# Kernel optimization log

Measured on AMD Instinct MI355X. Metric: run time of the kernel, lower is better.

## Reference

```python
import jax, jax.numpy as jnp
import numpy as np

EPS = 1e-6
NUM_HEADS = 16

def rmsnorm(x, w):
    # x: [..., d], w: [d]
    norm = jax.lax.rsqrt(jnp.mean(x * x, axis=-1, keepdims=True) + EPS)
    return w * (x * norm)

def setup_inputs() -> dict:
    key = jax.random.key(0)
    ks = jax.random.split(key, 6)
    B, N, C = 2, 2048, 1024
    H = NUM_HEADS
    hd = C // H
    x = jax.random.normal(ks[0], (B, N, C), dtype=jnp.float32)
    scale = 1.0 / np.sqrt(C)
    qkv_w = jax.random.normal(ks[1], (C, 3 * C), dtype=jnp.float32) * scale
    qkv_b = jnp.zeros((3 * C,), dtype=jnp.float32)
    q_norm_w = jnp.ones((hd,), dtype=jnp.float32)
    k_norm_w = jnp.ones((hd,), dtype=jnp.float32)
    proj_w = jax.random.normal(ks[2], (C, C), dtype=jnp.float32) * scale
    proj_b = jnp.zeros((C,), dtype=jnp.float32)
    return {"x": x, "qkv_w": qkv_w, "qkv_b": qkv_b,
            "q_norm_w": q_norm_w, "k_norm_w": k_norm_w,
            "proj_w": proj_w, "proj_b": proj_b}

def reference(x, qkv_w, qkv_b, q_norm_w, k_norm_w, proj_w, proj_b):
    B, N, C = x.shape
    H = NUM_HEADS
    hd = C // H
    qkv = x @ qkv_w + qkv_b                       # [B,N,3C]
    qkv = qkv.reshape(B, N, 3, H, hd)
    q, k, v = qkv[:, :, 0], qkv[:, :, 1], qkv[:, :, 2]  # [B,N,H,hd]
    q = jnp.transpose(q, (0, 2, 1, 3))            # [B,H,N,hd]
    k = jnp.transpose(k, (0, 2, 1, 3))
    v = jnp.transpose(v, (0, 2, 1, 3))
    q = rmsnorm(q, q_norm_w)
    k = rmsnorm(k, k_norm_w)
    scores = jnp.einsum('bhqd,bhkd->bhqk', q, k) / jnp.sqrt(jnp.float32(hd))
    attn = jax.nn.softmax(scores, axis=-1)
    out = jnp.einsum('bhqk,bhkd->bhqd', attn, v)  # [B,H,N,hd]
    out = jnp.transpose(out, (0, 2, 1, 3)).reshape(B, N, C)
    return out @ proj_w + proj_b
```

## Files before the change

kernel.cpp:

```cpp
#include <hip/hip_runtime.h>

typedef unsigned short u16;
typedef unsigned int u32;
typedef __bf16 bf16x8 __attribute__((ext_vector_type(8)));
typedef float f32x4 __attribute__((ext_vector_type(4)));
typedef unsigned short u16x8 __attribute__((ext_vector_type(8)));
typedef unsigned short u16x4 __attribute__((ext_vector_type(4)));
typedef float f4 __attribute__((ext_vector_type(4)));

__device__ __forceinline__ float bf2f(u16 u) {
    union { unsigned int i; float f; } c; c.i = ((unsigned int)u) << 16; return c.f;
}
__device__ __forceinline__ u16 f2bf(float f) {
    union { float f; unsigned int i; } c; c.f = f;
    unsigned int r = c.i + 0x7FFFu + ((c.i >> 16) & 1u);
    return (u16)(r >> 16);
}
__device__ __forceinline__ u16 f2bf_rtz(float f) {
    union { float f; unsigned int i; } c; c.f = f;
    return (u16)(c.i >> 16);
}
__device__ __forceinline__ float fast_exp2(float x) {
#if __has_builtin(__builtin_amdgcn_exp2f)
    return __builtin_amdgcn_exp2f(x);
#else
    return exp2f(x);
#endif
}
__device__ __forceinline__ void async16(const void* g, void* l) {
    __builtin_amdgcn_global_load_lds(
        (const __attribute__((address_space(1))) u32*)g,
        (__attribute__((address_space(3))) u32*)l, 16, 0, 0);
}

__global__ __launch_bounds__(256) void cast_bf16(
    const float* __restrict__ X, u16* __restrict__ H)
{
    const size_t i = ((size_t)blockIdx.x * 256 + threadIdx.x) * 8;
    u16x8 h;
    #pragma unroll
    for (int e = 0; e < 8; ++e) h[e] = f2bf(X[i + e]);
    *(u16x8*)&H[i] = h;
}

__global__ __launch_bounds__(256) void transpose_cast(
    const float* __restrict__ W, u16* __restrict__ Th, int K, int N)
{
    __shared__ float tile[32][33];
    const int bk = blockIdx.y * 32, bn = blockIdx.x * 32;
    const int tx = threadIdx.x & 31, ty = threadIdx.x >> 5;
    #pragma unroll
    for (int r = ty; r < 32; r += 8)
        tile[r][tx] = W[(size_t)(bk + r) * N + bn + tx];
    __syncthreads();
    #pragma unroll
    for (int r = ty; r < 32; r += 8)
        Th[(size_t)(bn + r) * K + bk + tx] = f2bf(tile[tx][r]);
}

__global__ __launch_bounds__(256) void gemm_qkv(
    const u16* __restrict__ AH, const u16* __restrict__ BH,
    const float* __restrict__ bias,
    u16* __restrict__ Qb, u16* __restrict__ Kb, u16* __restrict__ Vt,
    const float* __restrict__ qw, const float* __restrict__ kw)
{
    const int M = 4096, N = 3072, K = 1024; (void)M; (void)N;
    __shared__ __align__(16) u16 AhT[128 * 32];
    __shared__ __align__(16) u16 BhT[128 * 32];
    const int t = threadIdx.x;
    const int bm = blockIdx.y * 128, bn = blockIdx.x * 128;
    const int wave = t >> 6, lane = t & 63;
    const int wm = (wave >> 1) * 64, wn = (wave & 1) * 64;
    const int l15 = lane & 15, quad = lane >> 4;
    const int srow = lane >> 2, scol = (lane & 3) * 8;

    f32x4 acc[4][4];
    const f32x4 zero = {0.0f, 0.0f, 0.0f, 0.0f};
    #pragma unroll
    for (int i = 0; i < 4; ++i)
        #pragma unroll
        for (int j = 0; j < 4; ++j) acc[i][j] = zero;

    for (int k0 = 0; k0 < K; k0 += 32) {
        #pragma unroll
        for (int rr = 0; rr < 2; ++rr) {
            const int r0 = (rr * 4 + wave) * 16;
            const size_t ga = (size_t)(bm + r0 + srow) * K + k0 + scol;
            const size_t gb = (size_t)(bn + r0 + srow) * K + k0 + scol;
            async16(&AH[ga], &AhT[r0 * 32]);
            async16(&BH[gb], &BhT[r0 * 32]);
        }
        __syncthreads();
        bf16x8 ah[4], bh[4];
        #pragma unroll
        for (int i = 0; i < 4; ++i)
            ah[i] = *(const bf16x8*)&AhT[(wm + i * 16 + l15) * 32 + quad * 8];
        #pragma unroll
        for (int j = 0; j < 4; ++j)
            bh[j] = *(const bf16x8*)&BhT[(wn + j * 16 + l15) * 32 + quad * 8];
        #pragma unroll
        for (int i = 0; i < 4; ++i)
            #pragma unroll
            for (int j = 0; j < 4; ++j)
                acc[i][j] = __builtin_amdgcn_mfma_f32_16x16x32_bf16(
                    ah[i], bh[j], acc[i][j], 0, 0, 0);
        __syncthreads();
    }

    const int gc0 = bn + wn;
    const int sec = gc0 >> 10;
    const int h = (gc0 & 1023) >> 6;
    const int b = bm >> 11;
    const int bhd = b * 16 + h;
    float bv[4], wj[4];
    #pragma unroll
    for (int j = 0; j < 4; ++j) {
        const int d = j * 16 + l15;
        bv[j] = bias[gc0 + d];
        wj[j] = (sec == 2) ? 0.0f : (sec ? kw[d] : qw[d] * 0.18033688011f);
    }
    if (sec < 2) {
        u16* dst = sec ? Kb : Qb;
        #pragma unroll
        for (int i = 0; i < 4; ++i) {
            float val[4][4];
            float ss[4] = {0.0f, 0.0f, 0.0f, 0.0f};
            #pragma unroll
            for (int j = 0; j < 4; ++j)
                #pragma unroll
                for (int r = 0; r < 4; ++r) {
                    val[j][r] = acc[i][j][r] + bv[j];
                    ss[r] += val[j][r] * val[j][r];
                }
            #pragma unroll
            for (int r = 0; r < 4; ++r) {
                #pragma unroll
                for (int m = 1; m < 16; m <<= 1)
                    ss[r] += __shfl_xor(ss[r], m, 64);
                const float nrm = rsqrtf(ss[r] * 0.015625f + 1e-6f);
                const int n = (bm + wm + i * 16 + quad * 4 + r) & 2047;
                const size_t rowb = ((size_t)bhd * 2048 + n) * 64;
                #pragma unroll
                for (int j = 0; j < 4; ++j)
                    dst[rowb + j * 16 + l15] = f2bf(val[j][r] * nrm * wj[j]);
            }
        }
    } else {
        #pragma unroll
        for (int i = 0; i < 4; ++i) {
            const int n0 = (bm + wm + i * 16 + quad * 4) & 2047;
            #pragma unroll
            for (int j = 0; j < 4; ++j) {
                const int d = j * 16 + l15;
                u16x4 pk;
                #pragma unroll
                for (int r = 0; r < 4; ++r)
                    pk[r] = f2bf(acc[i][j][r] + bv[j]);
                *(u16x4*)&Vt[((size_t)bhd * 64 + d) * 2048 + n0] = pk;
            }
        }
    }
}

__global__ __launch_bounds__(256) void gemm_proj(
    const u16* __restrict__ AH, const u16* __restrict__ BH,
    const float* __restrict__ bias, float* __restrict__ C)
{
    const int N = 1024, K = 1024;
    __shared__ __align__(16) u16 AhT[64 * 32];
    __shared__ __align__(16) u16 BhT[128 * 32];
    const int t = threadIdx.x;
    const int bm = blockIdx.y * 64, bn = blockIdx.x * 128;
    const int wave = t >> 6, lane = t & 63;
    const int l15 = lane & 15, quad = lane >> 4;
    const int srow = lane >> 2, scol = (lane & 3) * 8;

    f32x4 acc[4][2];
    const f32x4 zero = {0.0f, 0.0f, 0.0f, 0.0f};
    #pragma unroll
    for (int i = 0; i < 4; ++i)
        #pragma unroll
        for (int j = 0; j < 2; ++j) acc[i][j] = zero;

    for (int k0 = 0; k0 < K; k0 += 32) {
        {
            const int r0 = wave * 16;
            async16(&AH[(size_t)(bm + r0 + srow) * K + k0 + scol],
                    &AhT[r0 * 32]);
        }
        #pragma unroll
        for (int cc = 0; cc < 2; ++cc) {
            const int r0 = (wave * 2 + cc) * 16;
            async16(&BH[(size_t)(bn + r0 + srow) * K + k0 + scol],
                    &BhT[r0 * 32]);
        }
        __syncthreads();
        bf16x8 ah[4], bh[2];
        #pragma unroll
        for (int i = 0; i < 4; ++i)
            ah[i] = *(const bf16x8*)&AhT[(i * 16 + l15) * 32 + quad * 8];
        #pragma unroll
        for (int j = 0; j < 2; ++j)
            bh[j] = *(const bf16x8*)
                &BhT[(wave * 32 + j * 16 + l15) * 32 + quad * 8];
        #pragma unroll
        for (int i = 0; i < 4; ++i)
            #pragma unroll
            for (int j = 0; j < 2; ++j)
                acc[i][j] = __builtin_amdgcn_mfma_f32_16x16x32_bf16(
                    ah[i], bh[j], acc[i][j], 0, 0, 0);
        __syncthreads();
    }

    #pragma unroll
    for (int j = 0; j < 2; ++j) {
        const int col = bn + wave * 32 + j * 16 + l15;
        const float bv = bias[col];
        #pragma unroll
        for (int i = 0; i < 4; ++i) {
            const int row = bm + i * 16 + quad * 4;
            #pragma unroll
            for (int r = 0; r < 4; ++r)
                C[(size_t)(row + r) * N + col] = acc[i][j][r] + bv;
        }
    }
}

__global__ __launch_bounds__(256) void flash_attn_mfma(
    const u16* __restrict__ Qb, const u16* __restrict__ Kb,
    const u16* __restrict__ Vt, float* __restrict__ Opart,
    float* __restrict__ Lpart)
{
    __shared__ __align__(16) u16 Qlds[128 * 64];
    __shared__ __align__(16) u16 Klds[64 * 64];
    __shared__ __align__(16) u16 Vlds[64 * 64];
    __shared__ u16 Plds[128][72];

    const int t = threadIdx.x;
    const int qt = blockIdx.x;
    const int bh = blockIdx.y;
    const int z = blockIdx.z;
    const int n0 = qt * 128;
    const size_t qbase = ((size_t)bh * 2048 + n0) * 64;
    const size_t kbase = (size_t)bh * 2048 * 64;
    const size_t vbase = (size_t)bh * 64 * 2048;
    const int wave = t >> 6, lane = t & 63;
    const int l15 = lane & 15, quad = lane >> 4;
    const int srow8 = lane >> 3;
    const int sgrp = lane & 7;

    #pragma unroll
    for (int c = 0; c < 4; ++c) {
        const int r0 = wave * 32 + c * 8;
        const int row = r0 + srow8;
        const int gg = sgrp ^ (row & 7);
        async16(&Qb[qbase + (size_t)row * 64 + gg * 8], &Qlds[r0 * 64]);
    }
    __syncthreads();

    int kofs[4][2];
    #pragma unroll
    for (int nt = 0; nt < 4; ++nt) {
        const int row = nt * 16 + l15;
        kofs[nt][0] = row * 64 + ((quad ^ (row & 7)) * 8);
        kofs[nt][1] = row * 64 + (((quad + 4) ^ (row & 7)) * 8);
    }
    bf16x8 qf[2][2];
    #pragma unroll
    for (int qs = 0; qs < 2; ++qs) {
        const int row = wave * 32 + qs * 16 + l15;
        qf[qs][0] = *(const bf16x8*)&Qlds[row * 64 + ((quad ^ (row & 7)) * 8)];
        qf[qs][1] = *(const bf16x8*)&Qlds[row * 64 + (((quad + 4) ^ (row & 7)) * 8)];
    }

    f32x4 o[2][4];
    const f32x4 zero = {0.0f, 0.0f, 0.0f, 0.0f};
    #pragma unroll
    for (int qs = 0; qs < 2; ++qs)
        #pragma unroll
        for (int dt = 0; dt < 4; ++dt) o[qs][dt] = zero;
    float lsum[2][4] = {};

    for (int kt = 0; kt < 16; ++kt) {
        const int ktG = z * 16 + kt;
        __syncthreads();
        #pragma unroll
        for (int cc = 0; cc < 2; ++cc) {
            const int r0 = (wave + cc * 4) * 8;
            const int row = r0 + srow8;
            const int gg = sgrp ^ (row & 7);
            async16(&Kb[kbase + (size_t)(ktG * 64 + row) * 64 + gg * 8],
                    &Klds[r0 * 64]);
            async16(&Vt[vbase + (size_t)row * 2048 + ktG * 64 + gg * 8],
                    &Vlds[r0 * 64]);
        }
        __syncthreads();

        f32x4 s[2][4];
        #pragma unroll
        for (int nt = 0; nt < 4; ++nt) {
            bf16x8 kf0 = *(const bf16x8*)&Klds[kofs[nt][0]];
            bf16x8 kf1 = *(const bf16x8*)&Klds[kofs[nt][1]];
            #pragma unroll
            for (int qs = 0; qs < 2; ++qs) {
                s[qs][nt] = zero;
                s[qs][nt] = __builtin_amdgcn_mfma_f32_16x16x32_bf16(
                    qf[qs][0], kf0, s[qs][nt], 0, 0, 0);
                s[qs][nt] = __builtin_amdgcn_mfma_f32_16x16x32_bf16(
                    qf[qs][1], kf1, s[qs][nt], 0, 0, 0);
            }
        }

        #pragma unroll
        for (int qs = 0; qs < 2; ++qs) {
            const int prow = wave * 32 + qs * 16 + quad * 4;
            #pragma unroll
            for (int nt = 0; nt < 4; ++nt)
                #pragma unroll
                for (int r = 0; r < 4; ++r) {
                    const float p = fast_exp2(s[qs][nt][r]);
                    lsum[qs][r] += p;
                    Plds[prow + r][nt * 16 + l15] = f2bf_rtz(p);
                }
        }

        bf16x8 pf[2][2];
        #pragma unroll
        for (int qs = 0; qs < 2; ++qs) {
            const int prow = wave * 32 + qs * 16 + l15;
            pf[qs][0] = *(const bf16x8*)&Plds[prow][quad * 8];
            pf[qs][1] = *(const bf16x8*)&Plds[prow][quad * 8 + 32];
        }

        #pragma unroll
        for (int dt = 0; dt < 4; ++dt) {
            bf16x8 vf0 = *(const bf16x8*)&Vlds[kofs[dt][0]];
            bf16x8 vf1 = *(const bf16x8*)&Vlds[kofs[dt][1]];
            #pragma unroll
            for (int qs = 0; qs < 2; ++qs) {
                o[qs][dt] = __builtin_amdgcn_mfma_f32_16x16x32_bf16(
                    pf[qs][0], vf0, o[qs][dt], 0, 0, 0);
                o[qs][dt] = __builtin_amdgcn_mfma_f32_16x16x32_bf16(
                    pf[qs][1], vf1, o[qs][dt], 0, 0, 0);
            }
        }
    }

    #pragma unroll
    for (int qs = 0; qs < 2; ++qs)
        #pragma unroll
        for (int r = 0; r < 4; ++r) {
            #pragma unroll
            for (int m = 1; m < 16; m <<= 1)
                lsum[qs][r] += __shfl_xor(lsum[qs][r], m, 64);
        }
    const int b = bh >> 4, h = bh & 15;
    const size_t obase =
        ((size_t)z * 4096 + b * 2048 + n0) * 1024 + h * 64;
    const size_t lbase = (size_t)z * 32 * 2048 + (size_t)bh * 2048 + n0;
    #pragma unroll
    for (int qs = 0; qs < 2; ++qs)
        #pragma unroll
        for (int r = 0; r < 4; ++r) {
            const int rofs = wave * 32 + qs * 16 + quad * 4 + r;
            if (l15 == 0) Lpart[lbase + rofs] = lsum[qs][r];
            const size_t rbase = obase + (size_t)rofs * 1024;
            #pragma unroll
            for (int dt = 0; dt < 4; ++dt)
                Opart[rbase + dt * 16 + l15] = o[qs][dt][r];
        }
}

__global__ __launch_bounds__(256) void attn_combine(
    const float* __restrict__ Opart, const float* __restrict__ Lpart,
    u16* __restrict__ Attn)
{
    const int row = blockIdx.x;
    const int t = threadIdx.x;
    const int col = t * 4;
    const int b = row >> 11, n = row & 2047;
    const int h = col >> 6;
    const int bh = b * 16 + h;
    const float l0 = Lpart[(size_t)bh * 2048 + n];
    const float l1 = Lpart[65536 + (size_t)bh * 2048 + n];
    const float inv = 1.0f / (l0 + l1);
    const size_t idx = (size_t)row * 1024 + col;
    f4 o0 = *(const f4*)&Opart[idx];
    f4 o1 = *(const f4*)&Opart[4194304 + idx];
    u16x4 pk;
    #pragma unroll
    for (int e = 0; e < 4; ++e) pk[e] = f2bf((o0[e] + o1[e]) * inv);
    *(u16x4*)&Attn[idx] = pk;
}

extern "C" void kernel_launch(void* const* d_in, const int* in_sizes, int n_in,
                              void* d_out, int out_size, void* d_ws, size_t ws_size,
                              hipStream_t stream)
{
    const float* x      = (const float*)d_in[0];
    const float* qkv_w  = (const float*)d_in[1];
    const float* qkv_b  = (const float*)d_in[2];
    const float* q_nw   = (const float*)d_in[3];
    const float* k_nw   = (const float*)d_in[4];
    const float* proj_w = (const float*)d_in[5];
    const float* proj_b = (const float*)d_in[6];
    float* out = (float*)d_out;

    char* ws = (char*)d_ws;
    u16* AttnB  = (u16*)ws;
    u16* qwT    = (u16*)(ws + 8388608);
    u16* pwT    = (u16*)(ws + 14680064);
    u16* Xb     = (u16*)(ws + 16777216);
    float* Lp   = (float*)(ws + 16777216);
    u16* QbB    = (u16*)(ws + 25165824);
    u16* KbB    = (u16*)(ws + 33554432);
    u16* VtB    = (u16*)(ws + 41943040);
    float* Op   = (float*)(ws + 50331648);
    (void)in_sizes; (void)n_in; (void)out_size;
    if (ws_size < 83886080u) return;

    cast_bf16<<<dim3(2048), 256, 0, stream>>>(x, Xb);
    transpose_cast<<<dim3(3072 / 32, 1024 / 32), 256, 0, stream>>>(
        qkv_w, qwT, 1024, 3072);
    transpose_cast<<<dim3(1024 / 32, 1024 / 32), 256, 0, stream>>>(
        proj_w, pwT, 1024, 1024);
    gemm_qkv<<<dim3(3072 / 128, 4096 / 128), 256, 0, stream>>>(
        Xb, qwT, qkv_b, QbB, KbB, VtB, q_nw, k_nw);
    flash_attn_mfma<<<dim3(16, 32, 2), 256, 0, stream>>>(
        QbB, KbB, VtB, Op, Lp);
    attn_combine<<<dim3(4096), 256, 0, stream>>>(Op, Lp, AttnB);
    gemm_proj<<<dim3(1024 / 128, 4096 / 64), 256, 0, stream>>>(
        AttnB, pwT, proj_b, out);
}
```

Before: 211.8 us.

## Drop split-K attention and fuse softmax normalization into flash kernel epilogue

The flash attention kernel no longer splits the key range across two z-blocks. Each block now walks all 32 key tiles and normalizes its output in the epilogue using row sums gathered through shared memory, then writes bf16 directly. This removes the fp32 partial-output writes, the Lpart buffer and the separate combine kernel launch. The QK MFMA operands are also swapped so each lane holds a full query row, which allows packed 4-wide P stores to LDS and a cheaper row-sum reduction. The cost is that the grid halves to 512 blocks, which reduces parallelism across CUs.

```diff
diff --git a/kernel.cpp b/kernel.cpp
--- a/kernel.cpp
+++ b/kernel.cpp
@@ -64,7 +64,7 @@
     u16* __restrict__ Qb, u16* __restrict__ Kb, u16* __restrict__ Vt,
     const float* __restrict__ qw, const float* __restrict__ kw)
 {
-    const int M = 4096, N = 3072, K = 1024; (void)M; (void)N;
+    const int K = 1024;
     __shared__ __align__(16) u16 AhT[128 * 32];
     __shared__ __align__(16) u16 BhT[128 * 32];
     const int t = threadIdx.x;
@@ -228,18 +228,17 @@
 
 __global__ __launch_bounds__(256) void flash_attn_mfma(
     const u16* __restrict__ Qb, const u16* __restrict__ Kb,
-    const u16* __restrict__ Vt, float* __restrict__ Opart,
-    float* __restrict__ Lpart)
+    const u16* __restrict__ Vt, u16* __restrict__ Attn)
 {
     __shared__ __align__(16) u16 Qlds[128 * 64];
     __shared__ __align__(16) u16 Klds[64 * 64];
     __shared__ __align__(16) u16 Vlds[64 * 64];
-    __shared__ u16 Plds[128][72];
+    __shared__ __align__(16) u16 Plds[128][72];
+    __shared__ float Lbuf[128];
 
     const int t = threadIdx.x;
     const int qt = blockIdx.x;
     const int bh = blockIdx.y;
-    const int z = blockIdx.z;
     const int n0 = qt * 128;
     const size_t qbase = ((size_t)bh * 2048 + n0) * 64;
     const size_t kbase = (size_t)bh * 2048 * 64;
@@ -279,19 +278,18 @@
     for (int qs = 0; qs < 2; ++qs)
         #pragma unroll
         for (int dt = 0; dt < 4; ++dt) o[qs][dt] = zero;
-    float lsum[2][4] = {};
-
-    for (int kt = 0; kt < 16; ++kt) {
-        const int ktG = z * 16 + kt;
+    float lsum[2] = {0.0f, 0.0f};
+
+    for (int kt = 0; kt < 32; ++kt) {
         __syncthreads();
         #pragma unroll
         for (int cc = 0; cc < 2; ++cc) {
             const int r0 = (wave + cc * 4) * 8;
             const int row = r0 + srow8;
             const int gg = sgrp ^ (row & 7);
-            async16(&Kb[kbase + (size_t)(ktG * 64 + row) * 64 + gg * 8],
+            async16(&Kb[kbase + (size_t)(kt * 64 + row) * 64 + gg * 8],
                     &Klds[r0 * 64]);
-            async16(&Vt[vbase + (size_t)row * 2048 + ktG * 64 + gg * 8],
+            async16(&Vt[vbase + (size_t)row * 2048 + kt * 64 + gg * 8],
                     &Vlds[r0 * 64]);
         }
         __syncthreads();
@@ -305,23 +303,26 @@
             for (int qs = 0; qs < 2; ++qs) {
                 s[qs][nt] = zero;
                 s[qs][nt] = __builtin_amdgcn_mfma_f32_16x16x32_bf16(
-                    qf[qs][0], kf0, s[qs][nt], 0, 0, 0);
+                    kf0, qf[qs][0], s[qs][nt], 0, 0, 0);
                 s[qs][nt] = __builtin_amdgcn_mfma_f32_16x16x32_bf16(
-                    qf[qs][1], kf1, s[qs][nt], 0, 0, 0);
+                    kf1, qf[qs][1], s[qs][nt], 0, 0, 0);
             }
         }
 
         #pragma unroll
         for (int qs = 0; qs < 2; ++qs) {
-            const int prow = wave * 32 + qs * 16 + quad * 4;
-            #pragma unroll
-            for (int nt = 0; nt < 4; ++nt)
+            const int prow = wave * 32 + qs * 16 + l15;
+            #pragma unroll
+            for (int nt = 0; nt < 4; ++nt) {
+                u16x4 pk;
                 #pragma unroll
                 for (int r = 0; r < 4; ++r) {
                     const float p = fast_exp2(s[qs][nt][r]);
-                    lsum[qs][r] += p;
-                    Plds[prow + r][nt * 16 + l15] = f2bf_rtz(p);
+                    lsum[qs] += p;
+                    pk[r] = f2bf_rtz(p);
                 }
+                *(u16x4*)&Plds[prow][nt * 16 + quad * 4] = pk;
+            }
         }
 
         bf16x8 pf[2][2];
@@ -347,50 +348,25 @@
     }
 
     #pragma unroll
+    for (int qs = 0; qs < 2; ++qs) {
+        lsum[qs] += __shfl_xor(lsum[qs], 16, 64);
+        lsum[qs] += __shfl_xor(lsum[qs], 32, 64);
+        if (quad == 0) Lbuf[wave * 32 + qs * 16 + l15] = lsum[qs];
+    }
+    const size_t obase =
+        ((size_t)(bh >> 4) * 2048 + n0) * 1024 + (bh & 15) * 64;
+    #pragma unroll
     for (int qs = 0; qs < 2; ++qs)
         #pragma unroll
         for (int r = 0; r < 4; ++r) {
-            #pragma unroll
-            for (int m = 1; m < 16; m <<= 1)
-                lsum[qs][r] += __shfl_xor(lsum[qs][r], m, 64);
-        }
-    const int b = bh >> 4, h = bh & 15;
-    const size_t obase =
-        ((size_t)z * 4096 + b * 2048 + n0) * 1024 + h * 64;
-    const size_t lbase = (size_t)z * 32 * 2048 + (size_t)bh * 2048 + n0;
-    #pragma unroll
-    for (int qs = 0; qs < 2; ++qs)
-        #pragma unroll
-        for (int r = 0; r < 4; ++r) {
-            const int rofs = wave * 32 + qs * 16 + quad * 4 + r;
-            if (l15 == 0) Lpart[lbase + rofs] = lsum[qs][r];
-            const size_t rbase = obase + (size_t)rofs * 1024;
+            const float inv =
+                1.0f / Lbuf[wave * 32 + qs * 16 + quad * 4 + r];
+            const size_t rbase =
+                obase + (size_t)(wave * 32 + qs * 16 + quad * 4 + r) * 1024;
             #pragma unroll
             for (int dt = 0; dt < 4; ++dt)
-                Opart[rbase + dt * 16 + l15] = o[qs][dt][r];
-        }
-}
-
-__global__ __launch_bounds__(256) void attn_combine(
-    const float* __restrict__ Opart, const float* __restrict__ Lpart,
-    u16* __restrict__ Attn)
-{
-    const int row = blockIdx.x;
-    const int t = threadIdx.x;
-    const int col = t * 4;
-    const int b = row >> 11, n = row & 2047;
-    const int h = col >> 6;
-    const int bh = b * 16 + h;
-    const float l0 = Lpart[(size_t)bh * 2048 + n];
-    const float l1 = Lpart[65536 + (size_t)bh * 2048 + n];
-    const float inv = 1.0f / (l0 + l1);
-    const size_t idx = (size_t)row * 1024 + col;
-    f4 o0 = *(const f4*)&Opart[idx];
-    f4 o1 = *(const f4*)&Opart[4194304 + idx];
-    u16x4 pk;
-    #pragma unroll
-    for (int e = 0; e < 4; ++e) pk[e] = f2bf((o0[e] + o1[e]) * inv);
-    *(u16x4*)&Attn[idx] = pk;
+                Attn[rbase + dt * 16 + l15] = f2bf(o[qs][dt][r] * inv);
+        }
 }
 
 extern "C" void kernel_launch(void* const* d_in, const int* in_sizes, int n_in,
@@ -407,17 +383,15 @@
     float* out = (float*)d_out;
 
     char* ws = (char*)d_ws;
-    u16* AttnB  = (u16*)ws;
-    u16* qwT    = (u16*)(ws + 8388608);
-    u16* pwT    = (u16*)(ws + 14680064);
-    u16* Xb     = (u16*)(ws + 16777216);
-    float* Lp   = (float*)(ws + 16777216);
-    u16* QbB    = (u16*)(ws + 25165824);
-    u16* KbB    = (u16*)(ws + 33554432);
-    u16* VtB    = (u16*)(ws + 41943040);
-    float* Op   = (float*)(ws + 50331648);
+    u16* AttnB = (u16*)ws;
+    u16* qwT   = (u16*)(ws + 8388608);
+    u16* pwT   = (u16*)(ws + 14680064);
+    u16* Xb    = (u16*)(ws + 16777216);
+    u16* QbB   = (u16*)(ws + 25165824);
+    u16* KbB   = (u16*)(ws + 33554432);
+    u16* VtB   = (u16*)(ws + 41943040);
     (void)in_sizes; (void)n_in; (void)out_size;
-    if (ws_size < 83886080u) return;
+    if (ws_size < 50331648u) return;
 
     cast_bf16<<<dim3(2048), 256, 0, stream>>>(x, Xb);
     transpose_cast<<<dim3(3072 / 32, 1024 / 32), 256, 0, stream>>>(
@@ -426,9 +400,7 @@
         proj_w, pwT, 1024, 1024);
     gemm_qkv<<<dim3(3072 / 128, 4096 / 128), 256, 0, stream>>>(
         Xb, qwT, qkv_b, QbB, KbB, VtB, q_nw, k_nw);
-    flash_attn_mfma<<<dim3(16, 32, 2), 256, 0, stream>>>(
-        QbB, KbB, VtB, Op, Lp);
-    attn_combine<<<dim3(4096), 256, 0, stream>>>(Op, Lp, AttnB);
+    flash_attn_mfma<<<dim3(16, 32), 256, 0, stream>>>(QbB, KbB, VtB, AttnB);
     gemm_proj<<<dim3(1024 / 128, 4096 / 64), 256, 0, stream>>>(
         AttnB, pwT, proj_b, out);
 }
```

Result: faster. 200.0 us (-5.6%).
